# Kernel optimization log

Measured on AMD Instinct MI355X. Metric: run time of the kernel, lower is better.

Reference implementation:

```python
import jax, jax.numpy as jnp
import numpy as np

NITERS = 5  # mean-field iterations (niters in __init__)


def setup_inputs() -> dict:
    key = jax.random.key(0)
    k1, k2 = jax.random.split(key)
    B, L, C, H, W = 2, 21, 3, 96, 96
    E0 = jax.random.normal(k1, (B, L, H, W), dtype=jnp.float32)
    Refs = jax.random.normal(k2, (B, C, H, W), dtype=jnp.float32)
    # potts_init: weight = ones(L,L) - eye(L)
    Mu_W = jnp.ones((L, L), dtype=jnp.float32) - jnp.eye(L, dtype=jnp.float32)
    return {"E0": E0, "Refs": Refs, "Mu_W": Mu_W}


def _affinity(Refs):
    # Reference-guided dense adjacency (BatchedAdjacency): row-normalized
    # Gaussian affinity on guide features, one N x N matrix per batch element.
    B, C, H, W = Refs.shape
    N = H * W
    f = Refs.reshape(B, C, N).transpose(0, 2, 1)  # [B, N, C]
    sq = jnp.sum(f * f, axis=-1)  # [B, N]
    D = sq[:, :, None] + sq[:, None, :] - 2.0 * jnp.einsum('bnc,bmc->bnm', f, f)
    A = jnp.exp(-0.5 * D)  # [B, N, N]
    return A / jnp.sum(A, axis=-1, keepdims=True)


def reference(E0, Refs, Mu_W):
    B, L, H, W = E0.shape
    N = H * W
    A = _affinity(Refs)  # computed once, reused every iteration
    E0f = E0.reshape(B, L, N)
    Qf = jax.nn.softmax(-E0f, axis=1)  # Q = softmax(-E0, dim=1)
    for _ in range(NITERS):
        # Potts compatibility transform (channel mixing): Mu(Q)
        M = jnp.einsum('kl,bln->bkn', Mu_W, Qf)
        # adjacency message passing: W(Mu(Q), Refs)
        msg = jnp.einsum('bnm,blm->bln', A, M)
        Qf = jax.nn.softmax(-(E0f + msg), axis=1)
    return Qf.reshape(B, L, H, W)
```

## Files before the change

### kernel.cpp

```cpp
#include <hip/hip_runtime.h>
#include <hip/hip_bf16.h>


#define BB 2
#define LL 21
#define LP (LL + 1)
#define NNPX 9216
#define NITERS 5
#define LOG2E 1.4426950408889634f

#define BARRIER() asm volatile("s_waitcnt lgkmcnt(0)\n\ts_barrier" ::: "memory")

typedef __attribute__((ext_vector_type(8))) short short8;
typedef __attribute__((ext_vector_type(4))) float f32x4;
typedef __attribute__((ext_vector_type(4))) unsigned int u32x4;

static __device__ inline unsigned int pk_bf16(float a, float b) {
    __hip_bfloat162 h = __float22bfloat162_rn(make_float2(a, b));
    unsigned int u;
    __builtin_memcpy(&u, &h, 4);
    return u;
}

__global__ __launch_bounds__(256) void k_prep(
        const float* __restrict__ E0, const float* __restrict__ Refs,
        const float* __restrict__ Mu,
        float4* __restrict__ FN, float4* __restrict__ FS,
        __hip_bfloat16* __restrict__ MQ) {
    __shared__ float muS[LL * LL];
    __shared__ float red1[4][64], red2[4][64];
    __shared__ float Qs[LL][64];

    int t = threadIdx.x;
    for (int i = t; i < LL * LL; i += 256) muS[i] = Mu[i];

    int q = t >> 6, px = t & 63;
    int pid = blockIdx.x * 64 + px;
    int b = pid / NNPX, n = pid % NNPX;

    if (q == 0) {
        const float* rb = Refs + (size_t)b * 3 * NNPX + n;
        float r0 = rb[0], r1 = rb[NNPX], r2 = rb[2 * NNPX];
        FN[pid] = make_float4(r0, r1, r2, 0.f);
        float g = -0.5f * (r0 * r0 + r1 * r1 + r2 * r2);
        FS[pid] = make_float4(g * LOG2E, r0 * LOG2E, r1 * LOG2E, r2 * LOG2E);
    }

    int l0 = q * 6;
    const float* eb = E0 + (size_t)b * LL * NNPX + n;
    float x[6];
    float mx = -1e30f;
    #pragma unroll
    for (int i = 0; i < 6; ++i) {
        int l = l0 + i;
        x[i] = (l < LL) ? -eb[(size_t)l * NNPX] : -1e30f;
        mx = fmaxf(mx, x[i]);
    }
    red1[q][px] = mx;
    __syncthreads();
    mx = fmaxf(fmaxf(red1[0][px], red1[1][px]), fmaxf(red1[2][px], red1[3][px]));
    float s = 0.f;
    #pragma unroll
    for (int i = 0; i < 6; ++i) { x[i] = __builtin_amdgcn_exp2f((x[i] - mx) * LOG2E); s += x[i]; }
    red2[q][px] = s;
    __syncthreads();
    float rs = __builtin_amdgcn_rcpf(red2[0][px] + red2[1][px] + red2[2][px] + red2[3][px]);
    #pragma unroll
    for (int i = 0; i < 6; ++i) if (l0 + i < LL) Qs[l0 + i][px] = x[i] * rs;
    __syncthreads();

    __hip_bfloat16* mq = MQ + (size_t)b * LL * NNPX + n;
    #pragma unroll
    for (int j = 0; j < 6; ++j) {
        int k = l0 + j;
        if (k < LL) {
            float a = 0.f;
            for (int l = 0; l < LL; ++l) a += muS[k * LL + l] * Qs[l][px];
            mq[(size_t)k * NNPX] = __float2bfloat16(a);
        }
    }
}

__global__ __launch_bounds__(256, 4) void k_accum(
        const float4* __restrict__ FS, const float4* __restrict__ FN,
        const unsigned int* __restrict__ MQbf, float* __restrict__ Ppart, int S) {
    __shared__ __align__(16) float FSlds[2][256];
    __shared__ __align__(16) unsigned short Mlds[2][32 * 64];

    int t = threadIdx.x;
    int rb = blockIdx.x;
    int s  = blockIdx.y;
    int b  = rb / 144;
    int n0 = (rb % 144) * 64;
    int wv = t >> 6, lane = t & 63;
    int lr = lane & 15, g = lane >> 4;

    for (int i = t; i < 11 * 32 * 2; i += 256) {
        int bufi = i >= 11 * 32;
        int ii = i - bufi * 11 * 32;
        int r = 21 + (ii >> 5), d = ii & 31;
        ((unsigned int*)&Mlds[bufi][r * 64])[d] = (r == 21) ? 0x3F803F80u : 0u;
    }

    int row = wv * 16 + lr;
    float4 fv = FN[b * NNPX + n0 + row];
    float fnx = fv.x, fny = fv.y, fnz = fv.z;

    const int T  = 144 / S;
    const int t0 = s * T;
    const float* fs32 = (const float*)(FS + (size_t)b * NNPX);
    const unsigned int* mqb = MQbf + (size_t)b * LL * (NNPX / 2);

    int mloc = t >> 2, comp = t & 3;
    int fslot = (mloc & ~7) | ((mloc ^ (mloc >> 3)) & 7);
    int fsw = fslot * 4 + comp;

    int sl0 = t >> 5, sm0 = t & 31;
    int sl1 = (t + 256) >> 5, sm1 = (t + 256) & 31;
    int sl2 = (t + 512) >> 5, sm2 = (t + 512) & 31;
    int mw0 = sl0 * 32 + (((sm0 >> 2) ^ (sl0 & 7)) << 2) + (sm0 & 3);
    int mw1 = sl1 * 32 + (((sm1 >> 2) ^ (sl1 & 7)) << 2) + (sm1 & 3);
    int mw2 = sl2 * 32 + (((sm2 >> 2) ^ (sl2 & 7)) << 2) + (sm2 & 3);

    int ib0 = lr * 64 + ((g ^ (lr & 7)) << 3);
    int ib1 = lr * 64 + (((g + 4) ^ (lr & 7)) << 3);
    int ib2 = (16 + lr) * 64 + ((g ^ (lr & 7)) << 3);
    int ib3 = (16 + lr) * 64 + (((g + 4) ^ (lr & 7)) << 3);

    f32x4 acc0 = {0.f, 0.f, 0.f, 0.f};
    f32x4 acc1 = {0.f, 0.f, 0.f, 0.f};

    int g8 = g * 8;

    float fsr;
    unsigned int mrA0, mrA1, mrA2;

    auto LOAD = [&](int tile) {
        int m0 = (t0 + tile) * 64;
        fsr = fs32[m0 * 4 + t];
        int mo0 = (t0 + tile) * 32;
        mrA0 = mqb[(size_t)sl0 * (NNPX / 2) + mo0 + sm0];
        mrA1 = mqb[(size_t)sl1 * (NNPX / 2) + mo0 + sm1];
        if (t < 160) mrA2 = mqb[(size_t)sl2 * (NNPX / 2) + mo0 + sm2];
    };
    auto STORE = [&](int buf) {
        FSlds[buf][fsw] = fsr;
        ((unsigned int*)Mlds[buf])[mw0] = mrA0;
        ((unsigned int*)Mlds[buf])[mw1] = mrA1;
        if (t < 160) ((unsigned int*)Mlds[buf])[mw2] = mrA2;
    };
    auto COMPUTE = [&](int buf) {
        const float4* FB = (const float4*)FSlds[buf];
        float w[8];
        #pragma unroll
        for (int j = 0; j < 8; ++j) {
            float4 F = FB[g8 + (j ^ g)];
            w[j] = __builtin_amdgcn_exp2f(F.x + fnx * F.y + fny * F.z + fnz * F.w);
        }
        u32x4 ap;
        #pragma unroll
        for (int j = 0; j < 4; ++j) ap[j] = pk_bf16(w[2 * j], w[2 * j + 1]);
        short8 a0 = __builtin_bit_cast(short8, ap);
        #pragma unroll
        for (int j = 0; j < 8; ++j) {
            float4 F = FB[32 + g8 + ((j ^ g) ^ 4)];
            w[j] = __builtin_amdgcn_exp2f(F.x + fnx * F.y + fny * F.z + fnz * F.w);
        }
        #pragma unroll
        for (int j = 0; j < 4; ++j) ap[j] = pk_bf16(w[2 * j], w[2 * j + 1]);
        short8 a1 = __builtin_bit_cast(short8, ap);

        short8 b00 = *(const short8*)&Mlds[buf][ib0];
        short8 b01 = *(const short8*)&Mlds[buf][ib1];
        short8 b10 = *(const short8*)&Mlds[buf][ib2];
        short8 b11 = *(const short8*)&Mlds[buf][ib3];
        acc0 = __builtin_amdgcn_mfma_f32_16x16x32_bf16(a0, b00, acc0, 0, 0, 0);
        acc0 = __builtin_amdgcn_mfma_f32_16x16x32_bf16(a1, b01, acc0, 0, 0, 0);
        acc1 = __builtin_amdgcn_mfma_f32_16x16x32_bf16(a0, b10, acc1, 0, 0, 0);
        acc1 = __builtin_amdgcn_mfma_f32_16x16x32_bf16(a1, b11, acc1, 0, 0, 0);
    };

    LOAD(0);
    STORE(0);
    BARRIER();

    for (int tt = 0; tt < T; ++tt) {
        int cur = tt & 1;
        if (tt + 1 < T) LOAD(tt + 1);
        COMPUTE(cur);
        if (tt + 1 < T) STORE(cur ^ 1);
        BARRIER();
    }

    int col = lane & 15, qr = lane >> 4;
    float* pp = Ppart + ((size_t)(s * BB + b) * LP) * NNPX;
    for (int r = 0; r < 4; ++r) {
        int n = n0 + wv * 16 + qr * 4 + r;
        pp[(size_t)col * NNPX + n] = acc0[r];
        if (col < LP - 16) pp[(size_t)(16 + col) * NNPX + n] = acc1[r];
    }
}

template <bool LAST>
__global__ __launch_bounds__(256) void k_softmax(
        const float* __restrict__ E0, const float* __restrict__ Ppart,
        const float* __restrict__ Mu,
        __hip_bfloat16* __restrict__ MQ, float* __restrict__ Out, int S) {
    __shared__ float muS[LL * LL];
    __shared__ float rsumS[64];
    __shared__ float red1[4][64], red2[4][64];
    __shared__ float Qs[LL][64];

    int t = threadIdx.x;
    if (!LAST) for (int i = t; i < LL * LL; i += 256) muS[i] = Mu[i];

    int q = t >> 6, px = t & 63;
    int pid = blockIdx.x * 64 + px;
    int b = pid / NNPX, n = pid % NNPX;

    int l0 = q * 6;
    const float* ppb = Ppart + n;
    const float* eb = E0 + (size_t)b * LL * NNPX + n;

    float Pa[6], e0v[6];
    #pragma unroll
    for (int i = 0; i < 6; ++i) {
        int l = l0 + i;
        Pa[i] = 0.f; e0v[i] = 0.f;
        if (l < LL) {
            for (int s = 0; s < S; ++s)
                Pa[i] += ppb[((size_t)(s * BB + b) * LP + l) * NNPX];
            e0v[i] = eb[(size_t)l * NNPX];
        }
    }
    if (q == 3) {
        float racc = 0.f;
        for (int s = 0; s < S; ++s)
            racc += ppb[((size_t)(s * BB + b) * LP + LL) * NNPX];
        rsumS[px] = racc;
    }
    __syncthreads();
    float rinv = __builtin_amdgcn_rcpf(rsumS[px]);

    float x[6];
    float mx = -1e30f;
    #pragma unroll
    for (int i = 0; i < 6; ++i) {
        x[i] = (l0 + i < LL) ? -(e0v[i] + Pa[i] * rinv) : -1e30f;
        mx = fmaxf(mx, x[i]);
    }
    red1[q][px] = mx;
    __syncthreads();
    mx = fmaxf(fmaxf(red1[0][px], red1[1][px]), fmaxf(red1[2][px], red1[3][px]));
    float ssum = 0.f;
    #pragma unroll
    for (int i = 0; i < 6; ++i) { x[i] = __builtin_amdgcn_exp2f((x[i] - mx) * LOG2E); ssum += x[i]; }
    red2[q][px] = ssum;
    __syncthreads();
    float rs = __builtin_amdgcn_rcpf(red2[0][px] + red2[1][px] + red2[2][px] + red2[3][px]);

    if (LAST) {
        float* ob = Out + (size_t)b * LL * NNPX + n;
        #pragma unroll
        for (int i = 0; i < 6; ++i) if (l0 + i < LL) ob[(size_t)(l0 + i) * NNPX] = x[i] * rs;
    } else {
        #pragma unroll
        for (int i = 0; i < 6; ++i) if (l0 + i < LL) Qs[l0 + i][px] = x[i] * rs;
        __syncthreads();
        __hip_bfloat16* mq = MQ + (size_t)b * LL * NNPX + n;
        #pragma unroll
        for (int j = 0; j < 6; ++j) {
            int k = l0 + j;
            if (k < LL) {
                float a = 0.f;
                for (int l = 0; l < LL; ++l) a += muS[k * LL + l] * Qs[l][px];
                mq[(size_t)k * NNPX] = __float2bfloat16(a);
            }
        }
    }
}

extern "C" void kernel_launch(void* const* d_in, const int* in_sizes, int n_in,
                              void* d_out, int out_size, void* d_ws, size_t ws_size,
                              hipStream_t stream) {
    const float* E0   = (const float*)d_in[0];
    const float* Refs = (const float*)d_in[1];
    const float* Mu   = (const float*)d_in[2];
    float* out = (float*)d_out;

    char* w = (char*)d_ws;
    size_t off = 0;
    auto alloc = [&](size_t bytes) {
        void* p = w + off;
        off += (bytes + 255) & ~(size_t)255;
        return p;
    };
    float4* FN     = (float4*)alloc((size_t)BB * NNPX * sizeof(float4));
    float4* FS     = (float4*)alloc((size_t)BB * NNPX * sizeof(float4));
    __hip_bfloat16* MQbf = (__hip_bfloat16*)alloc((size_t)BB * LL * NNPX * sizeof(__hip_bfloat16));

    size_t per = (size_t)BB * LP * NNPX * sizeof(float);
    size_t avail = ws_size > off ? ws_size - off : 0;
    int Smax = (int)(avail / (per + 256));
    static const int divs[] = {8, 6, 4, 3, 2, 1};
    int S = 1;
    for (int i = 0; i < 6; ++i) if (divs[i] <= Smax) { S = divs[i]; break; }
    float* Ppart = (float*)alloc((size_t)S * per);

    k_prep<<<BB * NNPX / 64, 256, 0, stream>>>(E0, Refs, Mu, FN, FS, MQbf);
    for (int it = 0; it < NITERS; ++it) {
        k_accum<<<dim3(288, S), 256, 0, stream>>>(FS, FN, (const unsigned int*)MQbf, Ppart, S);
        if (it == NITERS - 1)
            k_softmax<true><<<BB * NNPX / 64, 256, 0, stream>>>(E0, Ppart, Mu, MQbf, out, S);
        else
            k_softmax<false><<<BB * NNPX / 64, 256, 0, stream>>>(E0, Ppart, Mu, MQbf, out, S);
    }
}
```

Measured before the change: 370.9 us.

## Store Mu(Q) in MFMA-fragment tile layout and drop LDS staging in accumulate kernel

The producer kernels now write Mu(Q) in bf16 directly into a per-tile blob already arranged in MFMA B-operand fragment order, with the constant-one and zero padding columns written once in prep. The accumulate kernel then loads its B fragments straight from global memory into registers with register double-buffering. It also reads the source features directly from global memory instead of staging them in LDS, which removes all LDS traffic and barriers from its inner loop. In exchange, every wave reloads the same feature and fragment data from cache, and the producer writes become scattered 2-byte stores.

```diff
diff --git a/kernel.cpp b/kernel.cpp
--- a/kernel.cpp
+++ b/kernel.cpp
@@ -8,8 +8,9 @@
 #define NNPX 9216
 #define NITERS 5
 #define LOG2E 1.4426950408889634f
-
-#define BARRIER() asm volatile("s_waitcnt lgkmcnt(0)\n\ts_barrier" ::: "memory")
+#define INVL2E 0.6931471805599453f
+#define TILE_SH 2048
+#define BLOB_BATCH_SH (144 * TILE_SH)
 
 typedef __attribute__((ext_vector_type(8))) short short8;
 typedef __attribute__((ext_vector_type(4))) float f32x4;
@@ -22,11 +23,15 @@
     return u;
 }
 
+static __device__ inline int blob_off(int mm, int k) {
+    int base = ((mm >> 5) << 10) + (((mm >> 3) & 3) << 8) + ((mm & 7) << 1);
+    return (k < 16) ? base + (k << 4) : base + 2048 + ((k - 16) << 4);
+}
+
 __global__ __launch_bounds__(256) void k_prep(
         const float* __restrict__ E0, const float* __restrict__ Refs,
         const float* __restrict__ Mu,
-        float4* __restrict__ FN, float4* __restrict__ FS,
-        __hip_bfloat16* __restrict__ MQ) {
+        float4* __restrict__ FS, unsigned short* __restrict__ Blob) {
     __shared__ float muS[LL * LL];
     __shared__ float red1[4][64], red2[4][64];
     __shared__ float Qs[LL][64];
@@ -37,13 +42,22 @@
     int q = t >> 6, px = t & 63;
     int pid = blockIdx.x * 64 + px;
     int b = pid / NNPX, n = pid % NNPX;
+    int tile = blockIdx.x % 144;
+    unsigned short* tb = Blob + (size_t)b * BLOB_BATCH_SH + (size_t)tile * TILE_SH;
 
     if (q == 0) {
         const float* rb = Refs + (size_t)b * 3 * NNPX + n;
         float r0 = rb[0], r1 = rb[NNPX], r2 = rb[2 * NNPX];
-        FN[pid] = make_float4(r0, r1, r2, 0.f);
         float g = -0.5f * (r0 * r0 + r1 * r1 + r2 * r2);
         FS[pid] = make_float4(g * LOG2E, r0 * LOG2E, r1 * LOG2E, r2 * LOG2E);
+    }
+    if (t < 88) {
+        int f = 2 + (t >= 44);
+        int ii = t % 44;
+        int lane = (ii / 11) * 16 + 5 + (ii % 11);
+        unsigned int cv = (ii % 11 == 0) ? 0x3F803F80u : 0u;
+        u32x4 val = {cv, cv, cv, cv};
+        *(u32x4*)((char*)tb + f * 1024 + lane * 16) = val;
     }
 
     int l0 = q * 6;
@@ -69,133 +83,86 @@
     for (int i = 0; i < 6; ++i) if (l0 + i < LL) Qs[l0 + i][px] = x[i] * rs;
     __syncthreads();
 
-    __hip_bfloat16* mq = MQ + (size_t)b * LL * NNPX + n;
     #pragma unroll
     for (int j = 0; j < 6; ++j) {
         int k = l0 + j;
         if (k < LL) {
             float a = 0.f;
             for (int l = 0; l < LL; ++l) a += muS[k * LL + l] * Qs[l][px];
-            mq[(size_t)k * NNPX] = __float2bfloat16(a);
+            *(__hip_bfloat16*)((char*)tb + blob_off(px, k)) = __float2bfloat16(a);
         }
     }
 }
 
 __global__ __launch_bounds__(256, 4) void k_accum(
-        const float4* __restrict__ FS, const float4* __restrict__ FN,
-        const unsigned int* __restrict__ MQbf, float* __restrict__ Ppart, int S) {
-    __shared__ __align__(16) float FSlds[2][256];
-    __shared__ __align__(16) unsigned short Mlds[2][32 * 64];
-
+        const float4* __restrict__ FS, const unsigned short* __restrict__ Blob,
+        float* __restrict__ Ppart, int S) {
     int t = threadIdx.x;
     int rb = blockIdx.x;
     int s  = blockIdx.y;
     int b  = rb / 144;
-    int n0 = (rb % 144) * 64;
+    int n0b = (rb % 144) * 64;
     int wv = t >> 6, lane = t & 63;
     int lr = lane & 15, g = lane >> 4;
 
-    for (int i = t; i < 11 * 32 * 2; i += 256) {
-        int bufi = i >= 11 * 32;
-        int ii = i - bufi * 11 * 32;
-        int r = 21 + (ii >> 5), d = ii & 31;
-        ((unsigned int*)&Mlds[bufi][r * 64])[d] = (r == 21) ? 0x3F803F80u : 0u;
-    }
-
-    int row = wv * 16 + lr;
-    float4 fv = FN[b * NNPX + n0 + row];
-    float fnx = fv.x, fny = fv.y, fnz = fv.z;
-
     const int T  = 144 / S;
     const int t0 = s * T;
-    const float* fs32 = (const float*)(FS + (size_t)b * NNPX);
-    const unsigned int* mqb = MQbf + (size_t)b * LL * (NNPX / 2);
-
-    int mloc = t >> 2, comp = t & 3;
-    int fslot = (mloc & ~7) | ((mloc ^ (mloc >> 3)) & 7);
-    int fsw = fslot * 4 + comp;
-
-    int sl0 = t >> 5, sm0 = t & 31;
-    int sl1 = (t + 256) >> 5, sm1 = (t + 256) & 31;
-    int sl2 = (t + 512) >> 5, sm2 = (t + 512) & 31;
-    int mw0 = sl0 * 32 + (((sm0 >> 2) ^ (sl0 & 7)) << 2) + (sm0 & 3);
-    int mw1 = sl1 * 32 + (((sm1 >> 2) ^ (sl1 & 7)) << 2) + (sm1 & 3);
-    int mw2 = sl2 * 32 + (((sm2 >> 2) ^ (sl2 & 7)) << 2) + (sm2 & 3);
-
-    int ib0 = lr * 64 + ((g ^ (lr & 7)) << 3);
-    int ib1 = lr * 64 + (((g + 4) ^ (lr & 7)) << 3);
-    int ib2 = (16 + lr) * 64 + ((g ^ (lr & 7)) << 3);
-    int ib3 = (16 + lr) * 64 + (((g + 4) ^ (lr & 7)) << 3);
+    const float4* fsb = FS + (size_t)b * NNPX;
+    const unsigned short* blb = Blob + (size_t)b * BLOB_BATCH_SH;
+
+    float4 self = fsb[n0b + wv * 16 + lr];
+    float fnx = self.y * INVL2E, fny = self.z * INVL2E, fnz = self.w * INVL2E;
 
     f32x4 acc0 = {0.f, 0.f, 0.f, 0.f};
     f32x4 acc1 = {0.f, 0.f, 0.f, 0.f};
 
-    int g8 = g * 8;
-
-    float fsr;
-    unsigned int mrA0, mrA1, mrA2;
-
-    auto LOAD = [&](int tile) {
-        int m0 = (t0 + tile) * 64;
-        fsr = fs32[m0 * 4 + t];
-        int mo0 = (t0 + tile) * 32;
-        mrA0 = mqb[(size_t)sl0 * (NNPX / 2) + mo0 + sm0];
-        mrA1 = mqb[(size_t)sl1 * (NNPX / 2) + mo0 + sm1];
-        if (t < 160) mrA2 = mqb[(size_t)sl2 * (NNPX / 2) + mo0 + sm2];
+    auto LOADB = [&](int tile, short8& b0, short8& b1, short8& b2, short8& b3) {
+        const unsigned short* tp = blb + (size_t)(t0 + tile) * TILE_SH + lane * 8;
+        b0 = *(const short8*)(tp);
+        b1 = *(const short8*)(tp + 512);
+        b2 = *(const short8*)(tp + 1024);
+        b3 = *(const short8*)(tp + 1536);
     };
-    auto STORE = [&](int buf) {
-        FSlds[buf][fsw] = fsr;
-        ((unsigned int*)Mlds[buf])[mw0] = mrA0;
-        ((unsigned int*)Mlds[buf])[mw1] = mrA1;
-        if (t < 160) ((unsigned int*)Mlds[buf])[mw2] = mrA2;
+    auto GENA = [&](int tile, short8& a0, short8& a1) {
+        const float4* base = fsb + (size_t)(t0 + tile) * 64 + g * 8;
+        float w[8];
+        u32x4 ap;
+        #pragma unroll
+        for (int j = 0; j < 8; ++j) {
+            float4 F = base[j];
+            w[j] = __builtin_amdgcn_exp2f(F.x + fnx * F.y + fny * F.z + fnz * F.w);
+        }
+        #pragma unroll
+        for (int j = 0; j < 4; ++j) ap[j] = pk_bf16(w[2 * j], w[2 * j + 1]);
+        a0 = __builtin_bit_cast(short8, ap);
+        #pragma unroll
+        for (int j = 0; j < 8; ++j) {
+            float4 F = base[32 + j];
+            w[j] = __builtin_amdgcn_exp2f(F.x + fnx * F.y + fny * F.z + fnz * F.w);
+        }
+        #pragma unroll
+        for (int j = 0; j < 4; ++j) ap[j] = pk_bf16(w[2 * j], w[2 * j + 1]);
+        a1 = __builtin_bit_cast(short8, ap);
     };
-    auto COMPUTE = [&](int buf) {
-        const float4* FB = (const float4*)FSlds[buf];
-        float w[8];
-        #pragma unroll
-        for (int j = 0; j < 8; ++j) {
-            float4 F = FB[g8 + (j ^ g)];
-            w[j] = __builtin_amdgcn_exp2f(F.x + fnx * F.y + fny * F.z + fnz * F.w);
-        }
-        u32x4 ap;
-        #pragma unroll
-        for (int j = 0; j < 4; ++j) ap[j] = pk_bf16(w[2 * j], w[2 * j + 1]);
-        short8 a0 = __builtin_bit_cast(short8, ap);
-        #pragma unroll
-        for (int j = 0; j < 8; ++j) {
-            float4 F = FB[32 + g8 + ((j ^ g) ^ 4)];
-            w[j] = __builtin_amdgcn_exp2f(F.x + fnx * F.y + fny * F.z + fnz * F.w);
-        }
-        #pragma unroll
-        for (int j = 0; j < 4; ++j) ap[j] = pk_bf16(w[2 * j], w[2 * j + 1]);
-        short8 a1 = __builtin_bit_cast(short8, ap);
-
-        short8 b00 = *(const short8*)&Mlds[buf][ib0];
-        short8 b01 = *(const short8*)&Mlds[buf][ib1];
-        short8 b10 = *(const short8*)&Mlds[buf][ib2];
-        short8 b11 = *(const short8*)&Mlds[buf][ib3];
-        acc0 = __builtin_amdgcn_mfma_f32_16x16x32_bf16(a0, b00, acc0, 0, 0, 0);
-        acc0 = __builtin_amdgcn_mfma_f32_16x16x32_bf16(a1, b01, acc0, 0, 0, 0);
-        acc1 = __builtin_amdgcn_mfma_f32_16x16x32_bf16(a0, b10, acc1, 0, 0, 0);
-        acc1 = __builtin_amdgcn_mfma_f32_16x16x32_bf16(a1, b11, acc1, 0, 0, 0);
-    };
-
-    LOAD(0);
-    STORE(0);
-    BARRIER();
-
+
+    short8 c0, c1, c2, c3;
+    LOADB(0, c0, c1, c2, c3);
     for (int tt = 0; tt < T; ++tt) {
-        int cur = tt & 1;
-        if (tt + 1 < T) LOAD(tt + 1);
-        COMPUTE(cur);
-        if (tt + 1 < T) STORE(cur ^ 1);
-        BARRIER();
+        short8 p0, p1, p2, p3;
+        if (tt + 1 < T) LOADB(tt + 1, p0, p1, p2, p3);
+        short8 a0, a1;
+        GENA(tt, a0, a1);
+        acc0 = __builtin_amdgcn_mfma_f32_16x16x32_bf16(a0, c0, acc0, 0, 0, 0);
+        acc0 = __builtin_amdgcn_mfma_f32_16x16x32_bf16(a1, c1, acc0, 0, 0, 0);
+        acc1 = __builtin_amdgcn_mfma_f32_16x16x32_bf16(a0, c2, acc1, 0, 0, 0);
+        acc1 = __builtin_amdgcn_mfma_f32_16x16x32_bf16(a1, c3, acc1, 0, 0, 0);
+        c0 = p0; c1 = p1; c2 = p2; c3 = p3;
     }
 
     int col = lane & 15, qr = lane >> 4;
     float* pp = Ppart + ((size_t)(s * BB + b) * LP) * NNPX;
     for (int r = 0; r < 4; ++r) {
-        int n = n0 + wv * 16 + qr * 4 + r;
+        int n = n0b + wv * 16 + qr * 4 + r;
         pp[(size_t)col * NNPX + n] = acc0[r];
         if (col < LP - 16) pp[(size_t)(16 + col) * NNPX + n] = acc1[r];
     }
@@ -205,7 +172,7 @@
 __global__ __launch_bounds__(256) void k_softmax(
         const float* __restrict__ E0, const float* __restrict__ Ppart,
         const float* __restrict__ Mu,
-        __hip_bfloat16* __restrict__ MQ, float* __restrict__ Out, int S) {
+        unsigned short* __restrict__ Blob, float* __restrict__ Out, int S) {
     __shared__ float muS[LL * LL];
     __shared__ float rsumS[64];
     __shared__ float red1[4][64], red2[4][64];
@@ -217,6 +184,7 @@
     int q = t >> 6, px = t & 63;
     int pid = blockIdx.x * 64 + px;
     int b = pid / NNPX, n = pid % NNPX;
+    int tile = blockIdx.x % 144;
 
     int l0 = q * 6;
     const float* ppb = Ppart + n;
@@ -267,14 +235,14 @@
         #pragma unroll
         for (int i = 0; i < 6; ++i) if (l0 + i < LL) Qs[l0 + i][px] = x[i] * rs;
         __syncthreads();
-        __hip_bfloat16* mq = MQ + (size_t)b * LL * NNPX + n;
+        unsigned short* tb = Blob + (size_t)b * BLOB_BATCH_SH + (size_t)tile * TILE_SH;
         #pragma unroll
         for (int j = 0; j < 6; ++j) {
             int k = l0 + j;
             if (k < LL) {
                 float a = 0.f;
                 for (int l = 0; l < LL; ++l) a += muS[k * LL + l] * Qs[l][px];
-                mq[(size_t)k * NNPX] = __float2bfloat16(a);
+                *(__hip_bfloat16*)((char*)tb + blob_off(px, k)) = __float2bfloat16(a);
             }
         }
     }
@@ -295,9 +263,8 @@
         off += (bytes + 255) & ~(size_t)255;
         return p;
     };
-    float4* FN     = (float4*)alloc((size_t)BB * NNPX * sizeof(float4));
-    float4* FS     = (float4*)alloc((size_t)BB * NNPX * sizeof(float4));
-    __hip_bfloat16* MQbf = (__hip_bfloat16*)alloc((size_t)BB * LL * NNPX * sizeof(__hip_bfloat16));
+    float4* FS = (float4*)alloc((size_t)BB * NNPX * sizeof(float4));
+    unsigned short* Blob = (unsigned short*)alloc((size_t)BB * BLOB_BATCH_SH * sizeof(unsigned short));
 
     size_t per = (size_t)BB * LP * NNPX * sizeof(float);
     size_t avail = ws_size > off ? ws_size - off : 0;
@@ -307,12 +274,12 @@
     for (int i = 0; i < 6; ++i) if (divs[i] <= Smax) { S = divs[i]; break; }
     float* Ppart = (float*)alloc((size_t)S * per);
 
-    k_prep<<<BB * NNPX / 64, 256, 0, stream>>>(E0, Refs, Mu, FN, FS, MQbf);
+    k_prep<<<BB * NNPX / 64, 256, 0, stream>>>(E0, Refs, Mu, FS, Blob);
     for (int it = 0; it < NITERS; ++it) {
-        k_accum<<<dim3(288, S), 256, 0, stream>>>(FS, FN, (const unsigned int*)MQbf, Ppart, S);
+        k_accum<<<dim3(288, S), 256, 0, stream>>>(FS, Blob, Ppart, S);
         if (it == NITERS - 1)
-            k_softmax<true><<<BB * NNPX / 64, 256, 0, stream>>>(E0, Ppart, Mu, MQbf, out, S);
+            k_softmax<true><<<BB * NNPX / 64, 256, 0, stream>>>(E0, Ppart, Mu, Blob, out, S);
         else
-            k_softmax<false><<<BB * NNPX / 64, 256, 0, stream>>>(E0, Ppart, Mu, MQbf, out, S);
-    }
-}
+            k_softmax<false><<<BB * NNPX / 64, 256, 0, stream>>>(E0, Ppart, Mu, Blob, out, S);
+    }
+}
```

Result: slower. 615.4 us (+65.9%).

## Double rows per wave in accum, atomic-reduce splits into one buffer

Applied to the files above, without the earlier changes.

Each k_accum block now covers 128 query rows instead of 64, with each wave computing two 16-row MFMA tiles that share the same LDS-staged MQ B-fragments. This halves the count of staged tile loads per row and drops the FN buffer, recovering the row features from FS. The per-split partial buffers are replaced by float atomicAdd into a single zeroed accumulator (a memset each iteration), so the softmax kernel reads one buffer instead of summing S partials. The split count is fixed at 8. The costs are more exp work and registers per thread, atomic traffic, a memset launch per iteration, and nondeterministic summation order.

```diff
diff --git a/kernel.cpp b/kernel.cpp
--- a/kernel.cpp
+++ b/kernel.cpp
@@ -7,7 +7,9 @@
 #define LP (LL + 1)
 #define NNPX 9216
 #define NITERS 5
+#define MSPLIT 8
 #define LOG2E 1.4426950408889634f
+#define INVL2E 0.6931471805599453f
 
 #define BARRIER() asm volatile("s_waitcnt lgkmcnt(0)\n\ts_barrier" ::: "memory")
 
@@ -25,8 +27,7 @@
 __global__ __launch_bounds__(256) void k_prep(
         const float* __restrict__ E0, const float* __restrict__ Refs,
         const float* __restrict__ Mu,
-        float4* __restrict__ FN, float4* __restrict__ FS,
-        __hip_bfloat16* __restrict__ MQ) {
+        float4* __restrict__ FS, __hip_bfloat16* __restrict__ MQ) {
     __shared__ float muS[LL * LL];
     __shared__ float red1[4][64], red2[4][64];
     __shared__ float Qs[LL][64];
@@ -41,7 +42,6 @@
     if (q == 0) {
         const float* rb = Refs + (size_t)b * 3 * NNPX + n;
         float r0 = rb[0], r1 = rb[NNPX], r2 = rb[2 * NNPX];
-        FN[pid] = make_float4(r0, r1, r2, 0.f);
         float g = -0.5f * (r0 * r0 + r1 * r1 + r2 * r2);
         FS[pid] = make_float4(g * LOG2E, r0 * LOG2E, r1 * LOG2E, r2 * LOG2E);
     }
@@ -82,16 +82,16 @@
 }
 
 __global__ __launch_bounds__(256, 4) void k_accum(
-        const float4* __restrict__ FS, const float4* __restrict__ FN,
-        const unsigned int* __restrict__ MQbf, float* __restrict__ Ppart, int S) {
+        const float4* __restrict__ FS, const unsigned int* __restrict__ MQbf,
+        float* __restrict__ Ppart) {
     __shared__ __align__(16) float FSlds[2][256];
     __shared__ __align__(16) unsigned short Mlds[2][32 * 64];
 
     int t = threadIdx.x;
     int rb = blockIdx.x;
     int s  = blockIdx.y;
-    int b  = rb / 144;
-    int n0 = (rb % 144) * 64;
+    int b  = rb / 72;
+    int n0 = (rb % 72) * 128;
     int wv = t >> 6, lane = t & 63;
     int lr = lane & 15, g = lane >> 4;
 
@@ -102,14 +102,16 @@
         ((unsigned int*)&Mlds[bufi][r * 64])[d] = (r == 21) ? 0x3F803F80u : 0u;
     }
 
-    int row = wv * 16 + lr;
-    float4 fv = FN[b * NNPX + n0 + row];
-    float fnx = fv.x, fny = fv.y, fnz = fv.z;
-
-    const int T  = 144 / S;
+    const int T  = 144 / MSPLIT;
     const int t0 = s * T;
     const float* fs32 = (const float*)(FS + (size_t)b * NNPX);
+    const float4* fsb = FS + (size_t)b * NNPX;
     const unsigned int* mqb = MQbf + (size_t)b * LL * (NNPX / 2);
+
+    float4 sA = fsb[n0 + wv * 32 + lr];
+    float4 sB = fsb[n0 + wv * 32 + 16 + lr];
+    float fax = sA.y * INVL2E, fay = sA.z * INVL2E, faz = sA.w * INVL2E;
+    float fbx = sB.y * INVL2E, fby = sB.z * INVL2E, fbz = sB.w * INVL2E;
 
     int mloc = t >> 2, comp = t & 3;
     int fslot = (mloc & ~7) | ((mloc ^ (mloc >> 3)) & 7);
@@ -129,6 +131,8 @@
 
     f32x4 acc0 = {0.f, 0.f, 0.f, 0.f};
     f32x4 acc1 = {0.f, 0.f, 0.f, 0.f};
+    f32x4 acc2 = {0.f, 0.f, 0.f, 0.f};
+    f32x4 acc3 = {0.f, 0.f, 0.f, 0.f};
 
     int g8 = g * 8;
 
@@ -151,24 +155,34 @@
     };
     auto COMPUTE = [&](int buf) {
         const float4* FB = (const float4*)FSlds[buf];
-        float w[8];
+        float wA[8], wB[8];
+        u32x4 ap, cp;
         #pragma unroll
         for (int j = 0; j < 8; ++j) {
             float4 F = FB[g8 + (j ^ g)];
-            w[j] = __builtin_amdgcn_exp2f(F.x + fnx * F.y + fny * F.z + fnz * F.w);
-        }
-        u32x4 ap;
-        #pragma unroll
-        for (int j = 0; j < 4; ++j) ap[j] = pk_bf16(w[2 * j], w[2 * j + 1]);
+            wA[j] = __builtin_amdgcn_exp2f(F.x + fax * F.y + fay * F.z + faz * F.w);
+            wB[j] = __builtin_amdgcn_exp2f(F.x + fbx * F.y + fby * F.z + fbz * F.w);
+        }
+        #pragma unroll
+        for (int j = 0; j < 4; ++j) {
+            ap[j] = pk_bf16(wA[2 * j], wA[2 * j + 1]);
+            cp[j] = pk_bf16(wB[2 * j], wB[2 * j + 1]);
+        }
         short8 a0 = __builtin_bit_cast(short8, ap);
+        short8 c0 = __builtin_bit_cast(short8, cp);
         #pragma unroll
         for (int j = 0; j < 8; ++j) {
             float4 F = FB[32 + g8 + ((j ^ g) ^ 4)];
-            w[j] = __builtin_amdgcn_exp2f(F.x + fnx * F.y + fny * F.z + fnz * F.w);
-        }
-        #pragma unroll
-        for (int j = 0; j < 4; ++j) ap[j] = pk_bf16(w[2 * j], w[2 * j + 1]);
+            wA[j] = __builtin_amdgcn_exp2f(F.x + fax * F.y + fay * F.z + faz * F.w);
+            wB[j] = __builtin_amdgcn_exp2f(F.x + fbx * F.y + fby * F.z + fbz * F.w);
+        }
+        #pragma unroll
+        for (int j = 0; j < 4; ++j) {
+            ap[j] = pk_bf16(wA[2 * j], wA[2 * j + 1]);
+            cp[j] = pk_bf16(wB[2 * j], wB[2 * j + 1]);
+        }
         short8 a1 = __builtin_bit_cast(short8, ap);
+        short8 c1 = __builtin_bit_cast(short8, cp);
 
         short8 b00 = *(const short8*)&Mlds[buf][ib0];
         short8 b01 = *(const short8*)&Mlds[buf][ib1];
@@ -178,6 +192,10 @@
         acc0 = __builtin_amdgcn_mfma_f32_16x16x32_bf16(a1, b01, acc0, 0, 0, 0);
         acc1 = __builtin_amdgcn_mfma_f32_16x16x32_bf16(a0, b10, acc1, 0, 0, 0);
         acc1 = __builtin_amdgcn_mfma_f32_16x16x32_bf16(a1, b11, acc1, 0, 0, 0);
+        acc2 = __builtin_amdgcn_mfma_f32_16x16x32_bf16(c0, b00, acc2, 0, 0, 0);
+        acc2 = __builtin_amdgcn_mfma_f32_16x16x32_bf16(c1, b01, acc2, 0, 0, 0);
+        acc3 = __builtin_amdgcn_mfma_f32_16x16x32_bf16(c0, b10, acc3, 0, 0, 0);
+        acc3 = __builtin_amdgcn_mfma_f32_16x16x32_bf16(c1, b11, acc3, 0, 0, 0);
     };
 
     LOAD(0);
@@ -193,11 +211,15 @@
     }
 
     int col = lane & 15, qr = lane >> 4;
-    float* pp = Ppart + ((size_t)(s * BB + b) * LP) * NNPX;
+    float* pp = Ppart + (size_t)b * LP * NNPX;
     for (int r = 0; r < 4; ++r) {
-        int n = n0 + wv * 16 + qr * 4 + r;
-        pp[(size_t)col * NNPX + n] = acc0[r];
-        if (col < LP - 16) pp[(size_t)(16 + col) * NNPX + n] = acc1[r];
+        int nA = n0 + wv * 32 + qr * 4 + r;
+        atomicAdd(&pp[(size_t)col * NNPX + nA], acc0[r]);
+        atomicAdd(&pp[(size_t)col * NNPX + nA + 16], acc2[r]);
+        if (col < LP - 16) {
+            atomicAdd(&pp[(size_t)(16 + col) * NNPX + nA], acc1[r]);
+            atomicAdd(&pp[(size_t)(16 + col) * NNPX + nA + 16], acc3[r]);
+        }
     }
 }
 
@@ -205,9 +227,8 @@
 __global__ __launch_bounds__(256) void k_softmax(
         const float* __restrict__ E0, const float* __restrict__ Ppart,
         const float* __restrict__ Mu,
-        __hip_bfloat16* __restrict__ MQ, float* __restrict__ Out, int S) {
+        __hip_bfloat16* __restrict__ MQ, float* __restrict__ Out) {
     __shared__ float muS[LL * LL];
-    __shared__ float rsumS[64];
     __shared__ float red1[4][64], red2[4][64];
     __shared__ float Qs[LL][64];
 
@@ -219,34 +240,17 @@
     int b = pid / NNPX, n = pid % NNPX;
 
     int l0 = q * 6;
-    const float* ppb = Ppart + n;
+    const float* pp = Ppart + (size_t)b * LP * NNPX + n;
     const float* eb = E0 + (size_t)b * LL * NNPX + n;
-
-    float Pa[6], e0v[6];
+    float rinv = __builtin_amdgcn_rcpf(pp[(size_t)LL * NNPX]);
+
+    float x[6];
+    float mx = -1e30f;
     #pragma unroll
     for (int i = 0; i < 6; ++i) {
         int l = l0 + i;
-        Pa[i] = 0.f; e0v[i] = 0.f;
-        if (l < LL) {
-            for (int s = 0; s < S; ++s)
-                Pa[i] += ppb[((size_t)(s * BB + b) * LP + l) * NNPX];
-            e0v[i] = eb[(size_t)l * NNPX];
-        }
-    }
-    if (q == 3) {
-        float racc = 0.f;
-        for (int s = 0; s < S; ++s)
-            racc += ppb[((size_t)(s * BB + b) * LP + LL) * NNPX];
-        rsumS[px] = racc;
-    }
-    __syncthreads();
-    float rinv = __builtin_amdgcn_rcpf(rsumS[px]);
-
-    float x[6];
-    float mx = -1e30f;
-    #pragma unroll
-    for (int i = 0; i < 6; ++i) {
-        x[i] = (l0 + i < LL) ? -(e0v[i] + Pa[i] * rinv) : -1e30f;
+        x[i] = (l < LL) ? -(eb[(size_t)l * NNPX] + pp[(size_t)l * NNPX] * rinv)
+                        : -1e30f;
         mx = fmaxf(mx, x[i]);
     }
     red1[q][px] = mx;
@@ -295,24 +299,18 @@
         off += (bytes + 255) & ~(size_t)255;
         return p;
     };
-    float4* FN     = (float4*)alloc((size_t)BB * NNPX * sizeof(float4));
-    float4* FS     = (float4*)alloc((size_t)BB * NNPX * sizeof(float4));
+    float4* FS = (float4*)alloc((size_t)BB * NNPX * sizeof(float4));
     __hip_bfloat16* MQbf = (__hip_bfloat16*)alloc((size_t)BB * LL * NNPX * sizeof(__hip_bfloat16));
-
-    size_t per = (size_t)BB * LP * NNPX * sizeof(float);
-    size_t avail = ws_size > off ? ws_size - off : 0;
-    int Smax = (int)(avail / (per + 256));
-    static const int divs[] = {8, 6, 4, 3, 2, 1};
-    int S = 1;
-    for (int i = 0; i < 6; ++i) if (divs[i] <= Smax) { S = divs[i]; break; }
-    float* Ppart = (float*)alloc((size_t)S * per);
-
-    k_prep<<<BB * NNPX / 64, 256, 0, stream>>>(E0, Refs, Mu, FN, FS, MQbf);
+    size_t psz = (size_t)BB * LP * NNPX * sizeof(float);
+    float* Ppart = (float*)alloc(psz);
+
+    k_prep<<<BB * NNPX / 64, 256, 0, stream>>>(E0, Refs, Mu, FS, MQbf);
     for (int it = 0; it < NITERS; ++it) {
-        k_accum<<<dim3(288, S), 256, 0, stream>>>(FS, FN, (const unsigned int*)MQbf, Ppart, S);
+        hipMemsetAsync(Ppart, 0, psz, stream);
+        k_accum<<<dim3(144, MSPLIT), 256, 0, stream>>>(FS, (const unsigned int*)MQbf, Ppart);
         if (it == NITERS - 1)
-            k_softmax<true><<<BB * NNPX / 64, 256, 0, stream>>>(E0, Ppart, Mu, MQbf, out, S);
+            k_softmax<true><<<BB * NNPX / 64, 256, 0, stream>>>(E0, Ppart, Mu, MQbf, out);
         else
-            k_softmax<false><<<BB * NNPX / 64, 256, 0, stream>>>(E0, Ppart, Mu, MQbf, out, S);
-    }
-}
+            k_softmax<false><<<BB * NNPX / 64, 256, 0, stream>>>(E0, Ppart, Mu, MQbf, out);
+    }
+}
```

New measurement: 485.5 us. +30.9%, slower.
